# Kernel optimization log

Hardware: AMD Instinct MI355X
Metric: run time of the kernel (lower is better)

The kernel has to match this reference:

```python
import jax, jax.numpy as jnp
import numpy as np

B, L, E = 4, 2048, 1024
H, DH = 16, 64          # num_heads, head_dim; hidden = H*DH = 1024
HID = H * DH
EPS = 1e-5


def setup_inputs() -> dict:
    key = jax.random.key(0)
    ks = jax.random.split(key, 16)
    s = 0.02
    return {
        "emb": jax.random.normal(ks[0], (B, L, E), jnp.float32),
        "Wa": jax.random.normal(ks[1], (H, E, DH), jnp.float32) * s,
        "ba": jax.random.normal(ks[2], (H, DH), jnp.float32) * s,
        "Wb": jax.random.normal(ks[3], (H, E, DH), jnp.float32) * s,
        "bb": jax.random.normal(ks[4], (H, DH), jnp.float32) * s,
        "WD": jax.random.normal(ks[5], (H, E, DH), jnp.float32) * s,
        "bD": jax.random.normal(ks[6], (H, DH), jnp.float32) * s,
        "WC": jax.random.normal(ks[7], (H, DH, DH), jnp.float32) * s,
        "bC": jax.random.normal(ks[8], (H, DH), jnp.float32) * s,
        "ffn1_w": jax.random.normal(ks[9], (HID, 4 * HID), jnp.float32) * s,
        "ffn1_b": jnp.zeros((4 * HID,), jnp.float32),
        "ffn2_w": jax.random.normal(ks[10], (4 * HID, HID), jnp.float32) * s,
        "ffn2_b": jnp.zeros((HID,), jnp.float32),
        "proj_w": jax.random.normal(ks[11], (HID, HID), jnp.float32) * s,
        "proj_b": jnp.zeros((HID,), jnp.float32),
        "ln_g": jnp.ones((HID,), jnp.float32),
        "ln_b": jnp.zeros((HID,), jnp.float32),
    }


def _layernorm(x, g, b):
    mu = jnp.mean(x, -1, keepdims=True)
    var = jnp.mean(jnp.square(x - mu), -1, keepdims=True)
    return (x - mu) * jax.lax.rsqrt(var + EPS) * g + b


def reference(emb, Wa, ba, Wb, bb, WD, bD, WC, bC,
              ffn1_w, ffn1_b, ffn2_w, ffn2_b, proj_w, proj_b, ln_g, ln_b):
    # per-head gates/inputs for all timesteps at once: [B, L, H, DH]
    a = jnp.tanh(jnp.einsum('ble,hed->blhd', emb, Wa) + ba)
    b = jnp.einsum('ble,hed->blhd', emb, Wb) + bb

    # affine recurrence h_t = a_t * h_{t-1} + b_t, h_0 = 0 -> parallel scan over L
    def comb(c1, c2):
        a1, b1 = c1
        a2, b2 = c2
        return a1 * a2, a2 * b1 + b2

    _, h = jax.lax.associative_scan(comb, (a, b), axis=1)  # [B, L, H, DH]

    d = jnp.einsum('ble,hed->blhd', emb, WD) + bD
    head_out = (jnp.einsum('blhd,hdf->blhf', h, WC) + bC) * d  # [B, L, H, DH]
    z = head_out.reshape(B, L, HID)

    u = z + _layernorm(z, ln_g, ln_b)
    ffn = jax.nn.gelu(u @ ffn1_w + ffn1_b, approximate=False) @ ffn2_w + ffn2_b
    return (u + ffn) @ proj_w + proj_b
```

## Files before the change

### kernel.cpp

```cpp
#include <hip/hip_runtime.h>
#include <hip/hip_bf16.h>
#include <math.h>

#define B_   4
#define L_   2048
#define E_   1024
#define H_   16
#define DH_  64
#define HID_ 1024
#define ROWS (B_*L_)
#define NCH  16
#define CLEN (L_/NCH)

typedef __attribute__((ext_vector_type(8))) short short8;
typedef __attribute__((ext_vector_type(4))) float f32x4;

__device__ __forceinline__ unsigned short f2bf(float f) {
  union { float f; unsigned int i; } v; v.f = f;
  unsigned int r = v.i + 0x7fffu + ((v.i >> 16) & 1u);
  return (unsigned short)(r >> 16);
}
__device__ __forceinline__ float bf2f(unsigned int u) {
  union { unsigned int i; float f; } v; v.i = u << 16; return v.f;
}

__device__ __forceinline__ void gload16(const unsigned short* g, unsigned short* l) {
  __builtin_amdgcn_global_load_lds((const __attribute__((address_space(1))) void*)g,
                                   (__attribute__((address_space(3))) void*)l, 16, 0, 0);
}

__global__ void cast_f32_bf16(const float* __restrict__ src, unsigned short* __restrict__ dst, int n) {
  int i = (blockIdx.x * 256 + threadIdx.x) * 4;
  if (i < n) {
    float4 v = *(const float4*)(src + i);
    ushort4 o;
    o.x = f2bf(v.x); o.y = f2bf(v.y); o.z = f2bf(v.z); o.w = f2bf(v.w);
    *(ushort4*)(dst + i) = o;
  }
}

__global__ void transpose_cast(const float* __restrict__ src, unsigned short* __restrict__ dst,
                               int R, int C, int dstBase) {
  __shared__ float tile[32][33];
  src += (size_t)blockIdx.z * R * C;
  int dstRow0 = dstBase + blockIdx.z * C;
  int rb = blockIdx.x * 32, cb = blockIdx.y * 32;
  for (int i = threadIdx.y; i < 32; i += 8)
    tile[i][threadIdx.x] = src[(size_t)(rb + i) * C + cb + threadIdx.x];
  __syncthreads();
  for (int i = threadIdx.y; i < 32; i += 8)
    dst[(size_t)(dstRow0 + cb + i) * R + rb + threadIdx.x] = f2bf(tile[threadIdx.x][i]);
}

__global__ void build_bias(const float* __restrict__ ba, const float* __restrict__ bb,
                           const float* __restrict__ bD, float* __restrict__ bias) {
  int i = blockIdx.x * 256 + threadIdx.x;
  const float* src = (i < 1024) ? ba : ((i < 2048) ? bb : bD);
  bias[i] = src[i & 1023];
}

__global__ void build_wcd(const float* __restrict__ WC, unsigned short* __restrict__ dst) {
  int i = blockIdx.x * 256 + threadIdx.x;
  int c = i >> 7, kl = i & 127;
  float v = ((kl >> 6) == ((c >> 6) & 1)) ? WC[(size_t)(c >> 6) * 4096 + (kl & 63) * 64 + (c & 63)] : 0.f;
  dst[i] = f2bf(v);
}

#define EPI_GATES 0
#define EPI_GELU  1
#define EPI_RES   2
#define EPI_OUT   3
#define EPI_HEAD  4

template<int EPI>
__device__ __forceinline__ void epi_store(float xa, int rr, int cc, int N,
                                          const float* __restrict__ bias,
                                          const void* __restrict__ aux,
                                          void* __restrict__ out, void* __restrict__ out2) {
  float x = xa + bias[cc];
  if (EPI == EPI_GATES) {
    if (cc < HID_) {
      x = tanhf(x);
      ((unsigned short*)out)[(size_t)rr * 2048 + (cc << 1)] = f2bf(x);
    } else if (cc < 2048) {
      ((unsigned short*)out)[(size_t)rr * 2048 + ((cc - 1024) << 1) + 1] = f2bf(x);
    } else {
      ((unsigned short*)out2)[(size_t)rr * 1024 + (cc - 2048)] = f2bf(x);
    }
  } else if (EPI == EPI_GELU) {
    x = 0.5f * x * (1.f + erff(x * 0.70710678118654752f));
    ((unsigned short*)out)[(size_t)rr * N + cc] = f2bf(x);
  } else if (EPI == EPI_RES) {
    x += ((const float*)aux)[(size_t)rr * N + cc];
    ((unsigned short*)out)[(size_t)rr * N + cc] = f2bf(x);
  } else if (EPI == EPI_HEAD) {
    x *= bf2f(((const unsigned short*)aux)[(size_t)rr * 1024 + cc]);
    ((float*)out)[(size_t)rr * N + cc] = x;
  } else {
    ((float*)out)[(size_t)rr * N + cc] = x;
  }
}

template<int EPI, int DIAG>
__global__ __launch_bounds__(256)
void gemm_bt(const unsigned short* __restrict__ A, int lda,
             const unsigned short* __restrict__ Bt, int ldb,
             const float* __restrict__ bias, const void* __restrict__ aux,
             void* __restrict__ out, void* __restrict__ out2, int M, int N, int K) {
  __shared__ unsigned short lA[128 * 32];
  __shared__ unsigned short lB[128 * 32];
  const int tid = threadIdx.x;
  const int w = tid >> 6, l = tid & 63;
  const int gx = gridDim.x, nwg = gx * gridDim.y;
  const int o = blockIdx.y * gx + blockIdx.x;
  const int lin = (o & 7) * (nwg >> 3) + (o >> 3);
  const int row0 = (lin / gx) * 128, col0 = (lin % gx) * 128;
  const int kOff = DIAG ? col0 : 0;

  const int rA0 = w * 16 + (l >> 2);
  const int rA1 = (4 + w) * 16 + (l >> 2);
  const int koff = (l & 3) * 8;
  const unsigned short* gA0 = A + (size_t)(row0 + rA0) * lda + kOff + koff;
  const unsigned short* gA1 = A + (size_t)(row0 + rA1) * lda + kOff + koff;
  const unsigned short* gB0 = Bt + (size_t)(col0 + rA0) * ldb + koff;
  const unsigned short* gB1 = Bt + (size_t)(col0 + rA1) * ldb + koff;
  unsigned short* lA0 = lA + w * 512;
  unsigned short* lA1 = lA + (4 + w) * 512;
  unsigned short* lB0 = lB + w * 512;
  unsigned short* lB1 = lB + (4 + w) * 512;

  const int wr = (w >> 1) * 64, wc = (w & 1) * 64;
  f32x4 acc[4][4];
  #pragma unroll
  for (int m = 0; m < 4; m++)
    #pragma unroll
    for (int n = 0; n < 4; n++) acc[m][n] = (f32x4){0.f, 0.f, 0.f, 0.f};

  const int arow = wr + (l & 15);
  const int brow = wc + (l & 15);
  const int kg = (l >> 4) * 8;

  for (int kt = 0; kt < K; kt += 32) {
    __syncthreads();
    gload16(gA0 + kt, lA0);
    gload16(gA1 + kt, lA1);
    gload16(gB0 + kt, lB0);
    gload16(gB1 + kt, lB1);
    __syncthreads();
    short8 af[4], bfr[4];
    #pragma unroll
    for (int m = 0; m < 4; m++) af[m]  = *(const short8*)(lA + (arow + m * 16) * 32 + kg);
    #pragma unroll
    for (int n = 0; n < 4; n++) bfr[n] = *(const short8*)(lB + (brow + n * 16) * 32 + kg);
    #pragma unroll
    for (int m = 0; m < 4; m++)
      #pragma unroll
      for (int n = 0; n < 4; n++)
        acc[m][n] = __builtin_amdgcn_mfma_f32_16x16x32_bf16(af[m], bfr[n], acc[m][n], 0, 0, 0);
  }

  const int er = row0 + wr + ((l >> 4) << 2);
  const int ec = col0 + wc + (l & 15);
  #pragma unroll
  for (int m = 0; m < 4; m++)
    #pragma unroll
    for (int n = 0; n < 4; n++)
      #pragma unroll
      for (int j = 0; j < 4; j++)
        epi_store<EPI>(acc[m][n][j], er + m * 16 + j, ec + n * 16, N, bias, aux, out, out2);
}

template<int EPI>
__global__ __launch_bounds__(512, 2)
void gemm256(const unsigned short* __restrict__ A, const unsigned short* __restrict__ Bt,
             const float* __restrict__ bias, const void* __restrict__ aux,
             void* __restrict__ out, void* __restrict__ out2, int M, int N, int K) {
  __shared__ unsigned short lds[2][2][256 * 64];
  const int tid = threadIdx.x;
  const int w = tid >> 6, l = tid & 63;
  const int wm = w >> 2, wn = w & 3;
  const int gx = gridDim.x, nwg = gx * gridDim.y;
  const int o = blockIdx.y * gx + blockIdx.x;
  const int lin = (o & 7) * (nwg >> 3) + (o >> 3);
  const int row0 = (lin / gx) * 256, col0 = (lin % gx) * 256;
  const int lr = l & 15, kg = (l >> 4) << 3;
  const int wmb = wm * 128, wnb = wn * 64;
  const int nIter = K >> 7;

  const int srow = w * 8 + (l >> 3);
  const int kswz = (((l & 7) ^ (l >> 3)) << 3);

  f32x4 acc[8][4];
  #pragma unroll
  for (int m = 0; m < 8; m++)
    #pragma unroll
    for (int n = 0; n < 4; n++) acc[m][n] = (f32x4){0.f, 0.f, 0.f, 0.f};

  short8 a[4][2], b0[2][2], b1[2][2];

  auto stA = [&](int buf, int hh, int kt) {
    const unsigned short* g = A + (size_t)(row0 + hh * 128 + srow) * K + kt * 64 + kswz;
    unsigned short* d = &lds[buf][0][hh * 8192 + w * 512];
    gload16(g, d);
    gload16(g + (size_t)64 * K, d + 4096);
  };
  auto stB = [&](int buf, int hh, int kt) {
    const unsigned short* g = Bt + (size_t)(col0 + hh * 128 + srow) * K + kt * 64 + kswz;
    unsigned short* d = &lds[buf][1][hh * 8192 + w * 512];
    gload16(g, d);
    gload16(g + (size_t)64 * K, d + 4096);
  };

#define RD_A(LP, mh) { _Pragma("unroll") for (int mf = 0; mf < 4; ++mf) { _Pragma("unroll") for (int ks = 0; ks < 2; ++ks) { \
      int r = wmb + (mh) * 64 + mf * 16 + lr; int k = ks * 32 + kg; \
      a[mf][ks] = *(const short8*)((LP) + r * 64 + (k ^ ((r & 7) << 3))); } } }
#define RD_B(dst, LP, nh) { _Pragma("unroll") for (int nf = 0; nf < 2; ++nf) { _Pragma("unroll") for (int ks = 0; ks < 2; ++ks) { \
      int r = wnb + (nh) * 32 + nf * 16 + lr; int k = ks * 32 + kg; \
      dst[nf][ks] = *(const short8*)((LP) + r * 64 + (k ^ ((r & 7) << 3))); } } }
#define MMA(bb, MB, NB) \
    __builtin_amdgcn_s_setprio(1); \
    _Pragma("unroll") for (int mf = 0; mf < 4; ++mf) { _Pragma("unroll") for (int nf = 0; nf < 2; ++nf) { _Pragma("unroll") for (int ks = 0; ks < 2; ++ks) { \
      acc[(MB) + mf][(NB) + nf] = __builtin_amdgcn_mfma_f32_16x16x32_bf16(a[mf][ks], bb[nf][ks], acc[(MB) + mf][(NB) + nf], 0, 0, 0); } } } \
    __builtin_amdgcn_s_setprio(0);
#define BAR __builtin_amdgcn_s_barrier()

  stA(0, 0, 0); stA(0, 1, 0); stB(0, 0, 0); stB(0, 1, 0);
  stA(1, 0, 1); stA(1, 1, 1); stB(1, 0, 1); stB(1, 1, 1);
  asm volatile("s_waitcnt vmcnt(8)" ::: "memory");
  BAR;

  for (int i = 0; i < nIter; ++i) {
    const int t2 = 2 * i + 2, t3 = 2 * i + 3;
    const bool pf = (i + 1 < nIter);
    const unsigned short* LA0 = lds[0][0];
    const unsigned short* LB0 = lds[0][1];
    const unsigned short* LA1 = lds[1][0];
    const unsigned short* LB1 = lds[1][1];

    RD_A(LA0, 0); RD_B(b0, LB0, 0);
    BAR; MMA(b0, 0, 0); BAR;
    RD_B(b1, LB0, 1);
    BAR; MMA(b1, 0, 2); BAR;
    RD_A(LA0, 1);
    if (pf) { stB(0, 0, t2); stB(0, 1, t2); }
    BAR; MMA(b0, 4, 0); BAR;
    if (pf) { stA(0, 0, t2); stA(0, 1, t2);
              asm volatile("s_waitcnt vmcnt(8)" ::: "memory"); }
    else    { asm volatile("s_waitcnt vmcnt(0)" ::: "memory"); }
    BAR; MMA(b1, 4, 2); BAR;

    RD_A(LA1, 0); RD_B(b0, LB1, 0);
    BAR; MMA(b0, 0, 0); BAR;
    RD_B(b1, LB1, 1);
    BAR; MMA(b1, 0, 2); BAR;
    RD_A(LA1, 1);
    if (pf) { stB(1, 0, t3); stB(1, 1, t3); }
    BAR; MMA(b0, 4, 0); BAR;
    if (pf) { stA(1, 0, t3); stA(1, 1, t3);
              asm volatile("s_waitcnt vmcnt(8)" ::: "memory"); }
    BAR; MMA(b1, 4, 2); BAR;
  }
#undef RD_A
#undef RD_B
#undef MMA

  const int er = row0 + wmb + ((l >> 4) << 2);
  const int ec = col0 + wnb + lr;
  #pragma unroll
  for (int mi = 0; mi < 8; ++mi)
    #pragma unroll
    for (int ni = 0; ni < 4; ++ni)
      #pragma unroll
      for (int j = 0; j < 4; ++j)
        epi_store<EPI>(acc[mi][ni][j], er + mi * 16 + j, ec + ni * 16, N, bias, aux, out, out2);
}

template<int EPI>
__global__ __launch_bounds__(512, 2)
void gemm256x128(const unsigned short* __restrict__ A, const unsigned short* __restrict__ Bt,
                 const float* __restrict__ bias, const void* __restrict__ aux,
                 void* __restrict__ out, void* __restrict__ out2, int M, int N, int K) {
  __shared__ unsigned short lA2[2][256 * 64];
  __shared__ unsigned short lB2[2][128 * 64];
  const int tid = threadIdx.x;
  const int w = tid >> 6, l = tid & 63;
  const int wm = w >> 1, wn = w & 1;
  const int gx = gridDim.x, nwg = gx * gridDim.y;
  const int o = blockIdx.y * gx + blockIdx.x;
  const int lin = (o & 7) * (nwg >> 3) + (o >> 3);
  const int row0 = (lin / gx) * 256, col0 = (lin % gx) * 128;
  const int lr = l & 15, kg = (l >> 4) << 3;
  const int nIter = K >> 7;

  const int srow = w * 8 + (l >> 3);
  const int kswz = (((l & 7) ^ (l >> 3)) << 3);

  f32x4 acc[4][4];
  #pragma unroll
  for (int m = 0; m < 4; m++)
    #pragma unroll
    for (int n = 0; n < 4; n++) acc[m][n] = (f32x4){0.f, 0.f, 0.f, 0.f};

  short8 a[2][2], b0[2][2], b1[2][2];

  auto stA = [&](int buf, int hh, int kt) {
    const unsigned short* g = A + (size_t)(row0 + hh * 128 + srow) * K + kt * 64 + kswz;
    unsigned short* d = &lA2[buf][hh * 8192 + w * 512];
    gload16(g, d);
    gload16(g + (size_t)64 * K, d + 4096);
  };
  auto stB = [&](int buf, int hh, int kt) {
    const unsigned short* g = Bt + (size_t)(col0 + hh * 64 + srow) * K + kt * 64 + kswz;
    gload16(g, &lB2[buf][hh * 4096 + w * 512]);
  };

#define RDA2(buf, mh) { _Pragma("unroll") for (int mf = 0; mf < 2; ++mf) { _Pragma("unroll") for (int ks = 0; ks < 2; ++ks) { \
      int r = wm * 64 + (mh) * 32 + mf * 16 + lr; int k = ks * 32 + kg; \
      a[mf][ks] = *(const short8*)(&lA2[buf][r * 64 + (k ^ ((r & 7) << 3))]); } } }
#define RDB2(dst, buf, nh) { _Pragma("unroll") for (int nf = 0; nf < 2; ++nf) { _Pragma("unroll") for (int ks = 0; ks < 2; ++ks) { \
      int r = wn * 64 + (nh) * 32 + nf * 16 + lr; int k = ks * 32 + kg; \
      dst[nf][ks] = *(const short8*)(&lB2[buf][r * 64 + (k ^ ((r & 7) << 3))]); } } }
#define MMA2(bb, MB, NB) \
    __builtin_amdgcn_s_setprio(1); \
    _Pragma("unroll") for (int mf = 0; mf < 2; ++mf) { _Pragma("unroll") for (int nf = 0; nf < 2; ++nf) { _Pragma("unroll") for (int ks = 0; ks < 2; ++ks) { \
      acc[(MB) + mf][(NB) + nf] = __builtin_amdgcn_mfma_f32_16x16x32_bf16(a[mf][ks], bb[nf][ks], acc[(MB) + mf][(NB) + nf], 0, 0, 0); } } } \
    __builtin_amdgcn_s_setprio(0);
#define BAR2 __builtin_amdgcn_s_barrier()

  stA(0, 0, 0); stA(0, 1, 0); stB(0, 0, 0); stB(0, 1, 0);
  stA(1, 0, 1); stA(1, 1, 1); stB(1, 0, 1); stB(1, 1, 1);
  asm volatile("s_waitcnt vmcnt(6)" ::: "memory");
  BAR2;

  for (int i = 0; i < nIter; ++i) {
    const int t2 = 2 * i + 2, t3 = 2 * i + 3;
    const bool pf = (i + 1 < nIter);

    RDA2(0, 0); RDB2(b0, 0, 0);
    BAR2; MMA2(b0, 0, 0); BAR2;
    RDB2(b1, 0, 1);
    BAR2; MMA2(b1, 0, 2); BAR2;
    RDA2(0, 1);
    if (pf) { stB(0, 0, t2); stB(0, 1, t2); }
    BAR2; MMA2(b0, 2, 0); BAR2;
    if (pf) { stA(0, 0, t2); stA(0, 1, t2);
              asm volatile("s_waitcnt vmcnt(6)" ::: "memory"); }
    else    { asm volatile("s_waitcnt vmcnt(0)" ::: "memory"); }
    BAR2; MMA2(b1, 2, 2); BAR2;

    RDA2(1, 0); RDB2(b0, 1, 0);
    BAR2; MMA2(b0, 0, 0); BAR2;
    RDB2(b1, 1, 1);
    BAR2; MMA2(b1, 0, 2); BAR2;
    RDA2(1, 1);
    if (pf) { stB(1, 0, t3); stB(1, 1, t3); }
    BAR2; MMA2(b0, 2, 0); BAR2;
    if (pf) { stA(1, 0, t3); stA(1, 1, t3);
              asm volatile("s_waitcnt vmcnt(6)" ::: "memory"); }
    BAR2; MMA2(b1, 2, 2); BAR2;
  }
#undef RDA2
#undef RDB2
#undef MMA2

  const int er = row0 + wm * 64 + ((l >> 4) << 2);
  const int ec = col0 + wn * 64 + lr;
  #pragma unroll
  for (int mi = 0; mi < 4; ++mi)
    #pragma unroll
    for (int ni = 0; ni < 4; ++ni)
      #pragma unroll
      for (int j = 0; j < 4; ++j)
        epi_store<EPI>(acc[mi][ni][j], er + mi * 16 + j, ec + ni * 16, N, bias, aux, out, out2);
}

__global__ void scan_p1(const unsigned short* __restrict__ ab16, float* __restrict__ aggA, float* __restrict__ aggB) {
  int id = blockIdx.x * 256 + threadIdx.x;
  int c = id & 1023;
  int chunk = (id >> 10) & (NCH - 1);
  int bb = id >> 14;
  const unsigned short* base = ab16 + (size_t)(bb * L_ + chunk * CLEN) * 2048 + 2 * c;
  float Aa = 1.f, Bv = 0.f;
  #pragma unroll 4
  for (int t = 0; t < CLEN; ++t) {
    unsigned int v = *(const unsigned int*)(base + (size_t)t * 2048);
    float a = bf2f(v & 0xffffu);
    float b = bf2f(v >> 16);
    Aa *= a;
    Bv = a * Bv + b;
  }
  int o = (chunk * B_ + bb) * 1024 + c;
  aggA[o] = Aa; aggB[o] = Bv;
}

__global__ void scan_p2(const float* __restrict__ aggA, const float* __restrict__ aggB,
                        float* __restrict__ hinit) {
  int id = blockIdx.x * 256 + threadIdx.x;
  float hc = 0.f;
  for (int ch = 0; ch < NCH; ++ch) {
    int o = ch * 4096 + id;
    hinit[o] = hc;
    hc = aggA[o] * hc + aggB[o];
  }
}

__global__ void scan_p3(const unsigned short* __restrict__ ab16, const float* __restrict__ hinit,
                        unsigned short* __restrict__ hb16) {
  int id = blockIdx.x * 256 + threadIdx.x;
  int c = id & 1023;
  int chunk = (id >> 10) & (NCH - 1);
  int bb = id >> 14;
  const unsigned short* base = ab16 + (size_t)(bb * L_ + chunk * CLEN) * 2048 + 2 * c;
  unsigned short* hb = hb16 + (size_t)(bb * L_ + chunk * CLEN) * 1024;
  float h = hinit[chunk * 4096 + bb * 1024 + c];
  #pragma unroll 4
  for (int t = 0; t < CLEN; ++t) {
    unsigned int v = *(const unsigned int*)(base + (size_t)t * 2048);
    float a = bf2f(v & 0xffffu);
    float b = bf2f(v >> 16);
    h = a * h + b;
    hb[(size_t)t * 1024 + c] = f2bf(h);
  }
}

__global__ __launch_bounds__(256)
void ln_res(const float* __restrict__ z, const float* __restrict__ lg, const float* __restrict__ lb,
            float* __restrict__ u32, unsigned short* __restrict__ u16) {
  int row = blockIdx.x;
  int t = threadIdx.x;
  const float4 zv = *(const float4*)(z + (size_t)row * 1024 + t * 4);
  float s = zv.x + zv.y + zv.z + zv.w;
  float sq = zv.x * zv.x + zv.y * zv.y + zv.z * zv.z + zv.w * zv.w;
  #pragma unroll
  for (int o = 32; o > 0; o >>= 1) { s += __shfl_down(s, o); sq += __shfl_down(sq, o); }
  __shared__ float ps[4], pq[4];
  if ((t & 63) == 0) { ps[t >> 6] = s; pq[t >> 6] = sq; }
  __syncthreads();
  s = ps[0] + ps[1] + ps[2] + ps[3];
  sq = pq[0] + pq[1] + pq[2] + pq[3];
  float mu = s * (1.f / 1024.f);
  float var = sq * (1.f / 1024.f) - mu * mu;
  float rs = rsqrtf(var + 1e-5f);
  const float4 gv = *(const float4*)(lg + t * 4);
  const float4 bv = *(const float4*)(lb + t * 4);
  float4 o;
  o.x = zv.x + (zv.x - mu) * rs * gv.x + bv.x;
  o.y = zv.y + (zv.y - mu) * rs * gv.y + bv.y;
  o.z = zv.z + (zv.z - mu) * rs * gv.z + bv.z;
  o.w = zv.w + (zv.w - mu) * rs * gv.w + bv.w;
  *(float4*)(u32 + (size_t)row * 1024 + t * 4) = o;
  ushort4 ob; ob.x = f2bf(o.x); ob.y = f2bf(o.y); ob.z = f2bf(o.z); ob.w = f2bf(o.w);
  *(ushort4*)(u16 + (size_t)row * 1024 + t * 4) = ob;
}

extern "C" void kernel_launch(void* const* d_in, const int* in_sizes, int n_in,
                              void* d_out, int out_size, void* d_ws, size_t ws_size,
                              hipStream_t stream) {
  const float* emb    = (const float*)d_in[0];
  const float* Wa     = (const float*)d_in[1];
  const float* ba     = (const float*)d_in[2];
  const float* Wb     = (const float*)d_in[3];
  const float* bb     = (const float*)d_in[4];
  const float* WD     = (const float*)d_in[5];
  const float* bD     = (const float*)d_in[6];
  const float* WC     = (const float*)d_in[7];
  const float* bC     = (const float*)d_in[8];
  const float* ffn1_w = (const float*)d_in[9];
  const float* ffn1_b = (const float*)d_in[10];
  const float* ffn2_w = (const float*)d_in[11];
  const float* ffn2_b = (const float*)d_in[12];
  const float* proj_w = (const float*)d_in[13];
  const float* proj_b = (const float*)d_in[14];
  const float* ln_g   = (const float*)d_in[15];
  const float* ln_b   = (const float*)d_in[16];

  char* p = (char*)d_ws;
  auto alloc = [&](size_t bytes) { char* r = p; p += (bytes + 255) & ~(size_t)255; return (void*)r; };

  unsigned short* ab16 = (unsigned short*)alloc((size_t)ROWS * 2048 * 2);
  unsigned short* d16  = (unsigned short*)alloc((size_t)ROWS * 1024 * 2);
  unsigned short* hb16 = (unsigned short*)alloc((size_t)ROWS * 1024 * 2);
  float* zbuf  = (float*)alloc((size_t)ROWS * 1024 * 4);
  float* u32   = (float*)alloc((size_t)ROWS * 1024 * 4);
  unsigned short* u16  = (unsigned short*)alloc((size_t)ROWS * 1024 * 2);
  unsigned short* embb = (unsigned short*)alloc((size_t)ROWS * 1024 * 2);
  unsigned short* wcat = (unsigned short*)alloc((size_t)3072 * 1024 * 2);
  unsigned short* f1t  = (unsigned short*)alloc((size_t)4096 * 1024 * 2);
  unsigned short* f2t  = (unsigned short*)alloc((size_t)4096 * 1024 * 2);
  unsigned short* pjt  = (unsigned short*)alloc((size_t)1024 * 1024 * 2);
  unsigned short* wcd  = (unsigned short*)alloc((size_t)1024 * 128 * 2);
  float* biascat = (float*)alloc(3072 * 4);
  float* aggA  = (float*)alloc(65536 * 4);
  float* aggB  = (float*)alloc(65536 * 4);
  float* hinit = (float*)alloc(65536 * 4);
  unsigned short* gbuf = ab16;
  unsigned short* vbuf = (unsigned short*)zbuf;

  dim3 tb(32, 8);
  cast_f32_bf16<<<ROWS * 1024 / 1024, 256, 0, stream>>>(emb, embb, ROWS * 1024);
  build_bias<<<12, 256, 0, stream>>>(ba, bb, bD, biascat);
  build_wcd<<<1024 * 128 / 256, 256, 0, stream>>>(WC, wcd);
  transpose_cast<<<dim3(E_ / 32, DH_ / 32, H_), tb, 0, stream>>>(Wa, wcat, E_, DH_, 0);
  transpose_cast<<<dim3(E_ / 32, DH_ / 32, H_), tb, 0, stream>>>(Wb, wcat, E_, DH_, 1024);
  transpose_cast<<<dim3(E_ / 32, DH_ / 32, H_), tb, 0, stream>>>(WD, wcat, E_, DH_, 2048);
  transpose_cast<<<dim3(1024 / 32, 4096 / 32, 1), tb, 0, stream>>>(ffn1_w, f1t, 1024, 4096, 0);
  transpose_cast<<<dim3(4096 / 32, 1024 / 32, 1), tb, 0, stream>>>(ffn2_w, f2t, 4096, 1024, 0);
  transpose_cast<<<dim3(1024 / 32, 1024 / 32, 1), tb, 0, stream>>>(proj_w, pjt, 1024, 1024, 0);

  gemm256x128<EPI_GATES><<<dim3(3072 / 128, ROWS / 256), 512, 0, stream>>>(
      embb, wcat, biascat, nullptr, ab16, d16, ROWS, 3072, 1024);

  scan_p1<<<65536 / 256, 256, 0, stream>>>(ab16, aggA, aggB);
  scan_p2<<<4096 / 256, 256, 0, stream>>>(aggA, aggB, hinit);
  scan_p3<<<65536 / 256, 256, 0, stream>>>(ab16, hinit, hb16);

  gemm_bt<EPI_HEAD, 1><<<dim3(1024 / 128, ROWS / 128), 256, 0, stream>>>(
      hb16, 1024, wcd, 128, bC, d16, zbuf, nullptr, ROWS, 1024, 128);

  ln_res<<<ROWS, 256, 0, stream>>>(zbuf, ln_g, ln_b, u32, u16);

  gemm256<EPI_GELU><<<dim3(4096 / 256, ROWS / 256), 512, 0, stream>>>(
      u16, f1t, ffn1_b, nullptr, gbuf, nullptr, ROWS, 4096, 1024);
  gemm256x128<EPI_RES><<<dim3(1024 / 128, ROWS / 256), 512, 0, stream>>>(
      gbuf, f2t, ffn2_b, u32, vbuf, nullptr, ROWS, 1024, 4096);
  gemm256x128<EPI_OUT><<<dim3(1024 / 128, ROWS / 256), 512, 0, stream>>>(
      vbuf, pjt, proj_b, nullptr, (float*)d_out, nullptr, ROWS, 1024, 1024);
}
```

Baseline: 525.7 us.

## Simplify 256x256 GEMM pipeline and reroute smaller GEMMs to gemm_bt

Replaces the finely interleaved 256x256 GEMM schedule with a simpler loop. Each 64-wide K step loads all A/B fragments from LDS, runs all MFMAs, then prefetches two steps ahead with only two barriers per step. The gates GEMM now uses this 256x256 kernel instead of 256x128. The FFN2 and projection GEMMs move to the existing 128x128 gemm_bt kernel, and the 256x128 kernel is deleted. This cuts barrier count but loses the overlap of LDS reads, global prefetch and MFMA within a K step, and holds more fragment registers live.

Result: slower. 575.6 us (+9.5%).

```diff
diff --git a/kernel.cpp b/kernel.cpp
--- a/kernel.cpp
+++ b/kernel.cpp
@@ -172,9 +172,9 @@
 
 template<int EPI>
 __global__ __launch_bounds__(512, 2)
-void gemm256(const unsigned short* __restrict__ A, const unsigned short* __restrict__ Bt,
-             const float* __restrict__ bias, const void* __restrict__ aux,
-             void* __restrict__ out, void* __restrict__ out2, int M, int N, int K) {
+void gemm256v2(const unsigned short* __restrict__ A, const unsigned short* __restrict__ Bt,
+               const float* __restrict__ bias, const void* __restrict__ aux,
+               void* __restrict__ out, void* __restrict__ out2, int M, int N, int K) {
   __shared__ unsigned short lds[2][2][256 * 64];
   const int tid = threadIdx.x;
   const int w = tid >> 6, l = tid & 63;
@@ -185,7 +185,7 @@
   const int row0 = (lin / gx) * 256, col0 = (lin % gx) * 256;
   const int lr = l & 15, kg = (l >> 4) << 3;
   const int wmb = wm * 128, wnb = wn * 64;
-  const int nIter = K >> 7;
+  const int nT = K >> 6;
 
   const int srow = w * 8 + (l >> 3);
   const int kswz = (((l & 7) ^ (l >> 3)) << 3);
@@ -196,177 +196,93 @@
     #pragma unroll
     for (int n = 0; n < 4; n++) acc[m][n] = (f32x4){0.f, 0.f, 0.f, 0.f};
 
-  short8 a[4][2], b0[2][2], b1[2][2];
-
-  auto stA = [&](int buf, int hh, int kt) {
-    const unsigned short* g = A + (size_t)(row0 + hh * 128 + srow) * K + kt * 64 + kswz;
-    unsigned short* d = &lds[buf][0][hh * 8192 + w * 512];
-    gload16(g, d);
-    gload16(g + (size_t)64 * K, d + 4096);
+  auto stage = [&](int buf, int kt) {
+    const unsigned short* ga = A + (size_t)(row0 + srow) * K + kt * 64 + kswz;
+    const unsigned short* gb = Bt + (size_t)(col0 + srow) * K + kt * 64 + kswz;
+    unsigned short* da = &lds[buf][0][w * 512];
+    unsigned short* db = &lds[buf][1][w * 512];
+    gload16(ga, da);
+    gload16(ga + (size_t)64 * K, da + 4096);
+    gload16(ga + (size_t)128 * K, da + 8192);
+    gload16(ga + (size_t)192 * K, da + 12288);
+    gload16(gb, db);
+    gload16(gb + (size_t)64 * K, db + 4096);
+    gload16(gb + (size_t)128 * K, db + 8192);
+    gload16(gb + (size_t)192 * K, db + 12288);
   };
-  auto stB = [&](int buf, int hh, int kt) {
-    const unsigned short* g = Bt + (size_t)(col0 + hh * 128 + srow) * K + kt * 64 + kswz;
-    unsigned short* d = &lds[buf][1][hh * 8192 + w * 512];
-    gload16(g, d);
-    gload16(g + (size_t)64 * K, d + 4096);
-  };
-
-#define RD_A(LP, mh) { _Pragma("unroll") for (int mf = 0; mf < 4; ++mf) { _Pragma("unroll") for (int ks = 0; ks < 2; ++ks) { \
-      int r = wmb + (mh) * 64 + mf * 16 + lr; int k = ks * 32 + kg; \
-      a[mf][ks] = *(const short8*)((LP) + r * 64 + (k ^ ((r & 7) << 3))); } } }
-#define RD_B(dst, LP, nh) { _Pragma("unroll") for (int nf = 0; nf < 2; ++nf) { _Pragma("unroll") for (int ks = 0; ks < 2; ++ks) { \
-      int r = wnb + (nh) * 32 + nf * 16 + lr; int k = ks * 32 + kg; \
-      dst[nf][ks] = *(const short8*)((LP) + r * 64 + (k ^ ((r & 7) << 3))); } } }
-#define MMA(bb, MB, NB) \
-    __builtin_amdgcn_s_setprio(1); \
-    _Pragma("unroll") for (int mf = 0; mf < 4; ++mf) { _Pragma("unroll") for (int nf = 0; nf < 2; ++nf) { _Pragma("unroll") for (int ks = 0; ks < 2; ++ks) { \
-      acc[(MB) + mf][(NB) + nf] = __builtin_amdgcn_mfma_f32_16x16x32_bf16(a[mf][ks], bb[nf][ks], acc[(MB) + mf][(NB) + nf], 0, 0, 0); } } } \
+
+  stage(0, 0);
+  stage(1, 1);
+  asm volatile("s_waitcnt vmcnt(8)" ::: "memory");
+  __builtin_amdgcn_s_barrier();
+
+  for (int t = 0; t < nT; ++t) {
+    const int buf = t & 1;
+    const unsigned short* LA = lds[buf][0];
+    const unsigned short* LB = lds[buf][1];
+
+    short8 fa0[4][2], fa1[4][2], fb[2][2][2];
+    #pragma unroll
+    for (int nh = 0; nh < 2; ++nh)
+      #pragma unroll
+      for (int nf = 0; nf < 2; ++nf)
+        #pragma unroll
+        for (int ks = 0; ks < 2; ++ks) {
+          int r = wnb + nh * 32 + nf * 16 + lr; int k = ks * 32 + kg;
+          fb[nh][nf][ks] = *(const short8*)(LB + r * 64 + (k ^ ((r & 7) << 3)));
+        }
+    #pragma unroll
+    for (int mf = 0; mf < 4; ++mf)
+      #pragma unroll
+      for (int ks = 0; ks < 2; ++ks) {
+        int r = wmb + mf * 16 + lr; int k = ks * 32 + kg;
+        fa0[mf][ks] = *(const short8*)(LA + r * 64 + (k ^ ((r & 7) << 3)));
+      }
+    #pragma unroll
+    for (int mf = 0; mf < 4; ++mf)
+      #pragma unroll
+      for (int ks = 0; ks < 2; ++ks) {
+        int r = wmb + 64 + mf * 16 + lr; int k = ks * 32 + kg;
+        fa1[mf][ks] = *(const short8*)(LA + r * 64 + (k ^ ((r & 7) << 3)));
+      }
+
+    __builtin_amdgcn_s_setprio(1);
+    #pragma unroll
+    for (int nh = 0; nh < 2; ++nh)
+      #pragma unroll
+      for (int nf = 0; nf < 2; ++nf)
+        #pragma unroll
+        for (int mf = 0; mf < 4; ++mf)
+          #pragma unroll
+          for (int ks = 0; ks < 2; ++ks)
+            acc[mf][nh * 2 + nf] = __builtin_amdgcn_mfma_f32_16x16x32_bf16(
+                fa0[mf][ks], fb[nh][nf][ks], acc[mf][nh * 2 + nf], 0, 0, 0);
+    #pragma unroll
+    for (int nh = 0; nh < 2; ++nh)
+      #pragma unroll
+      for (int nf = 0; nf < 2; ++nf)
+        #pragma unroll
+        for (int mf = 0; mf < 4; ++mf)
+          #pragma unroll
+          for (int ks = 0; ks < 2; ++ks)
+            acc[4 + mf][nh * 2 + nf] = __builtin_amdgcn_mfma_f32_16x16x32_bf16(
+                fa1[mf][ks], fb[nh][nf][ks], acc[4 + mf][nh * 2 + nf], 0, 0, 0);
     __builtin_amdgcn_s_setprio(0);
-#define BAR __builtin_amdgcn_s_barrier()
-
-  stA(0, 0, 0); stA(0, 1, 0); stB(0, 0, 0); stB(0, 1, 0);
-  stA(1, 0, 1); stA(1, 1, 1); stB(1, 0, 1); stB(1, 1, 1);
-  asm volatile("s_waitcnt vmcnt(8)" ::: "memory");
-  BAR;
-
-  for (int i = 0; i < nIter; ++i) {
-    const int t2 = 2 * i + 2, t3 = 2 * i + 3;
-    const bool pf = (i + 1 < nIter);
-    const unsigned short* LA0 = lds[0][0];
-    const unsigned short* LB0 = lds[0][1];
-    const unsigned short* LA1 = lds[1][0];
-    const unsigned short* LB1 = lds[1][1];
-
-    RD_A(LA0, 0); RD_B(b0, LB0, 0);
-    BAR; MMA(b0, 0, 0); BAR;
-    RD_B(b1, LB0, 1);
-    BAR; MMA(b1, 0, 2); BAR;
-    RD_A(LA0, 1);
-    if (pf) { stB(0, 0, t2); stB(0, 1, t2); }
-    BAR; MMA(b0, 4, 0); BAR;
-    if (pf) { stA(0, 0, t2); stA(0, 1, t2);
-              asm volatile("s_waitcnt vmcnt(8)" ::: "memory"); }
-    else    { asm volatile("s_waitcnt vmcnt(0)" ::: "memory"); }
-    BAR; MMA(b1, 4, 2); BAR;
-
-    RD_A(LA1, 0); RD_B(b0, LB1, 0);
-    BAR; MMA(b0, 0, 0); BAR;
-    RD_B(b1, LB1, 1);
-    BAR; MMA(b1, 0, 2); BAR;
-    RD_A(LA1, 1);
-    if (pf) { stB(1, 0, t3); stB(1, 1, t3); }
-    BAR; MMA(b0, 4, 0); BAR;
-    if (pf) { stA(1, 0, t3); stA(1, 1, t3);
-              asm volatile("s_waitcnt vmcnt(8)" ::: "memory"); }
-    BAR; MMA(b1, 4, 2); BAR;
-  }
-#undef RD_A
-#undef RD_B
-#undef MMA
+
+    __builtin_amdgcn_s_barrier();
+    if (t + 2 < nT) {
+      stage(buf, t + 2);
+      asm volatile("s_waitcnt vmcnt(8)" ::: "memory");
+    } else {
+      asm volatile("s_waitcnt vmcnt(0)" ::: "memory");
+    }
+    __builtin_amdgcn_s_barrier();
+  }
 
   const int er = row0 + wmb + ((l >> 4) << 2);
   const int ec = col0 + wnb + lr;
   #pragma unroll
   for (int mi = 0; mi < 8; ++mi)
-    #pragma unroll
-    for (int ni = 0; ni < 4; ++ni)
-      #pragma unroll
-      for (int j = 0; j < 4; ++j)
-        epi_store<EPI>(acc[mi][ni][j], er + mi * 16 + j, ec + ni * 16, N, bias, aux, out, out2);
-}
-
-template<int EPI>
-__global__ __launch_bounds__(512, 2)
-void gemm256x128(const unsigned short* __restrict__ A, const unsigned short* __restrict__ Bt,
-                 const float* __restrict__ bias, const void* __restrict__ aux,
-                 void* __restrict__ out, void* __restrict__ out2, int M, int N, int K) {
-  __shared__ unsigned short lA2[2][256 * 64];
-  __shared__ unsigned short lB2[2][128 * 64];
-  const int tid = threadIdx.x;
-  const int w = tid >> 6, l = tid & 63;
-  const int wm = w >> 1, wn = w & 1;
-  const int gx = gridDim.x, nwg = gx * gridDim.y;
-  const int o = blockIdx.y * gx + blockIdx.x;
-  const int lin = (o & 7) * (nwg >> 3) + (o >> 3);
-  const int row0 = (lin / gx) * 256, col0 = (lin % gx) * 128;
-  const int lr = l & 15, kg = (l >> 4) << 3;
-  const int nIter = K >> 7;
-
-  const int srow = w * 8 + (l >> 3);
-  const int kswz = (((l & 7) ^ (l >> 3)) << 3);
-
-  f32x4 acc[4][4];
-  #pragma unroll
-  for (int m = 0; m < 4; m++)
-    #pragma unroll
-    for (int n = 0; n < 4; n++) acc[m][n] = (f32x4){0.f, 0.f, 0.f, 0.f};
-
-  short8 a[2][2], b0[2][2], b1[2][2];
-
-  auto stA = [&](int buf, int hh, int kt) {
-    const unsigned short* g = A + (size_t)(row0 + hh * 128 + srow) * K + kt * 64 + kswz;
-    unsigned short* d = &lA2[buf][hh * 8192 + w * 512];
-    gload16(g, d);
-    gload16(g + (size_t)64 * K, d + 4096);
-  };
-  auto stB = [&](int buf, int hh, int kt) {
-    const unsigned short* g = Bt + (size_t)(col0 + hh * 64 + srow) * K + kt * 64 + kswz;
-    gload16(g, &lB2[buf][hh * 4096 + w * 512]);
-  };
-
-#define RDA2(buf, mh) { _Pragma("unroll") for (int mf = 0; mf < 2; ++mf) { _Pragma("unroll") for (int ks = 0; ks < 2; ++ks) { \
-      int r = wm * 64 + (mh) * 32 + mf * 16 + lr; int k = ks * 32 + kg; \
-      a[mf][ks] = *(const short8*)(&lA2[buf][r * 64 + (k ^ ((r & 7) << 3))]); } } }
-#define RDB2(dst, buf, nh) { _Pragma("unroll") for (int nf = 0; nf < 2; ++nf) { _Pragma("unroll") for (int ks = 0; ks < 2; ++ks) { \
-      int r = wn * 64 + (nh) * 32 + nf * 16 + lr; int k = ks * 32 + kg; \
-      dst[nf][ks] = *(const short8*)(&lB2[buf][r * 64 + (k ^ ((r & 7) << 3))]); } } }
-#define MMA2(bb, MB, NB) \
-    __builtin_amdgcn_s_setprio(1); \
-    _Pragma("unroll") for (int mf = 0; mf < 2; ++mf) { _Pragma("unroll") for (int nf = 0; nf < 2; ++nf) { _Pragma("unroll") for (int ks = 0; ks < 2; ++ks) { \
-      acc[(MB) + mf][(NB) + nf] = __builtin_amdgcn_mfma_f32_16x16x32_bf16(a[mf][ks], bb[nf][ks], acc[(MB) + mf][(NB) + nf], 0, 0, 0); } } } \
-    __builtin_amdgcn_s_setprio(0);
-#define BAR2 __builtin_amdgcn_s_barrier()
-
-  stA(0, 0, 0); stA(0, 1, 0); stB(0, 0, 0); stB(0, 1, 0);
-  stA(1, 0, 1); stA(1, 1, 1); stB(1, 0, 1); stB(1, 1, 1);
-  asm volatile("s_waitcnt vmcnt(6)" ::: "memory");
-  BAR2;
-
-  for (int i = 0; i < nIter; ++i) {
-    const int t2 = 2 * i + 2, t3 = 2 * i + 3;
-    const bool pf = (i + 1 < nIter);
-
-    RDA2(0, 0); RDB2(b0, 0, 0);
-    BAR2; MMA2(b0, 0, 0); BAR2;
-    RDB2(b1, 0, 1);
-    BAR2; MMA2(b1, 0, 2); BAR2;
-    RDA2(0, 1);
-    if (pf) { stB(0, 0, t2); stB(0, 1, t2); }
-    BAR2; MMA2(b0, 2, 0); BAR2;
-    if (pf) { stA(0, 0, t2); stA(0, 1, t2);
-              asm volatile("s_waitcnt vmcnt(6)" ::: "memory"); }
-    else    { asm volatile("s_waitcnt vmcnt(0)" ::: "memory"); }
-    BAR2; MMA2(b1, 2, 2); BAR2;
-
-    RDA2(1, 0); RDB2(b0, 1, 0);
-    BAR2; MMA2(b0, 0, 0); BAR2;
-    RDB2(b1, 1, 1);
-    BAR2; MMA2(b1, 0, 2); BAR2;
-    RDA2(1, 1);
-    if (pf) { stB(1, 0, t3); stB(1, 1, t3); }
-    BAR2; MMA2(b0, 2, 0); BAR2;
-    if (pf) { stA(1, 0, t3); stA(1, 1, t3);
-              asm volatile("s_waitcnt vmcnt(6)" ::: "memory"); }
-    BAR2; MMA2(b1, 2, 2); BAR2;
-  }
-#undef RDA2
-#undef RDB2
-#undef MMA2
-
-  const int er = row0 + wm * 64 + ((l >> 4) << 2);
-  const int ec = col0 + wn * 64 + lr;
-  #pragma unroll
-  for (int mi = 0; mi < 4; ++mi)
     #pragma unroll
     for (int ni = 0; ni < 4; ++ni)
       #pragma unroll
@@ -507,7 +423,7 @@
   transpose_cast<<<dim3(4096 / 32, 1024 / 32, 1), tb, 0, stream>>>(ffn2_w, f2t, 4096, 1024, 0);
   transpose_cast<<<dim3(1024 / 32, 1024 / 32, 1), tb, 0, stream>>>(proj_w, pjt, 1024, 1024, 0);
 
-  gemm256x128<EPI_GATES><<<dim3(3072 / 128, ROWS / 256), 512, 0, stream>>>(
+  gemm256v2<EPI_GATES><<<dim3(3072 / 256, ROWS / 256), 512, 0, stream>>>(
       embb, wcat, biascat, nullptr, ab16, d16, ROWS, 3072, 1024);
 
   scan_p1<<<65536 / 256, 256, 0, stream>>>(ab16, aggA, aggB);
@@ -519,10 +435,10 @@
 
   ln_res<<<ROWS, 256, 0, stream>>>(zbuf, ln_g, ln_b, u32, u16);
 
-  gemm256<EPI_GELU><<<dim3(4096 / 256, ROWS / 256), 512, 0, stream>>>(
+  gemm256v2<EPI_GELU><<<dim3(4096 / 256, ROWS / 256), 512, 0, stream>>>(
       u16, f1t, ffn1_b, nullptr, gbuf, nullptr, ROWS, 4096, 1024);
-  gemm256x128<EPI_RES><<<dim3(1024 / 128, ROWS / 256), 512, 0, stream>>>(
-      gbuf, f2t, ffn2_b, u32, vbuf, nullptr, ROWS, 1024, 4096);
-  gemm256x128<EPI_OUT><<<dim3(1024 / 128, ROWS / 256), 512, 0, stream>>>(
-      vbuf, pjt, proj_b, nullptr, (float*)d_out, nullptr, ROWS, 1024, 1024);
-}
+  gemm_bt<EPI_RES, 0><<<dim3(1024 / 128, ROWS / 128), 256, 0, stream>>>(
+      gbuf, 4096, f2t, 4096, ffn2_b, u32, vbuf, nullptr, ROWS, 1024, 4096);
+  gemm_bt<EPI_OUT, 0><<<dim3(1024 / 128, ROWS / 128), 256, 0, stream>>>(
+      vbuf, 1024, pjt, 1024, proj_b, nullptr, (float*)d_out, nullptr, ROWS, 1024, 1024);
+}
```
